# Performance work log

Hardware: AMD Instinct MI355X
Metric: run time of the kernel (lower is better)

## Reference

```python
import jax, jax.numpy as jnp
import numpy as np

POOL = 7
IMG_H, IMG_W = 1024, 1024
CANONICAL = 224.0  # canonical box size used in the FPN level assignment


def _crop_and_resize(fm, boxes, ph, pw):
    """TF-style crop_and_resize (extrapolation_value=0).

    fm: [C, H, W] feature map; boxes: [N, 4] normalized (y1, x1, y2, x2).
    Returns [N, C, ph, pw] bilinearly sampled crops.
    """
    C, H, W = fm.shape
    y1, x1, y2, x2 = boxes[:, 0], boxes[:, 1], boxes[:, 2], boxes[:, 3]
    ty = jnp.arange(ph, dtype=boxes.dtype) / (ph - 1)  # [ph] in [0,1]
    tx = jnp.arange(pw, dtype=boxes.dtype) / (pw - 1)
    ys = (y1[:, None] + (y2 - y1)[:, None] * ty) * (H - 1)  # [N, ph] image coords
    xs = (x1[:, None] + (x2 - x1)[:, None] * tx) * (W - 1)  # [N, pw]
    yy = jnp.broadcast_to(ys[:, :, None], (ys.shape[0], ph, pw))  # [N, ph, pw]
    xx = jnp.broadcast_to(xs[:, None, :], (xs.shape[0], ph, pw))
    y0f = jnp.floor(yy)
    x0f = jnp.floor(xx)
    wy = yy - y0f
    wx = xx - x0f
    y0 = jnp.clip(y0f.astype(jnp.int32), 0, H - 1)
    y1i = jnp.clip(y0 + 1, 0, H - 1)
    x0 = jnp.clip(x0f.astype(jnp.int32), 0, W - 1)
    x1i = jnp.clip(x0 + 1, 0, W - 1)

    def g(yi, xi):
        return fm[:, yi, xi]  # [C, N, ph, pw]

    val = (g(y0, x0) * ((1 - wy) * (1 - wx))[None]
           + g(y0, x1i) * ((1 - wy) * wx)[None]
           + g(y1i, x0) * (wy * (1 - wx))[None]
           + g(y1i, x1i) * (wy * wx)[None])
    # extrapolation_value = 0 for samples outside the feature map
    inb = (yy >= 0) & (yy <= H - 1) & (xx >= 0) & (xx <= W - 1)
    val = jnp.where(inb[None], val, 0.0)
    return jnp.transpose(val, (1, 0, 2, 3))  # [N, C, ph, pw]


def setup_inputs() -> dict:
    key = jax.random.key(0)
    k1, k2, k3, k4, k5, k6, k7, k8 = jax.random.split(key, 8)
    N = 1000
    y1 = jax.random.uniform(k1, (N, 1)) * 0.7
    x1 = jax.random.uniform(k2, (N, 1)) * 0.7
    hh = jax.random.uniform(k3, (N, 1)) * 0.28 + 0.02
    ww = jax.random.uniform(k4, (N, 1)) * 0.28 + 0.02
    boxes = jnp.concatenate([y1, x1, y1 + hh, x1 + ww], axis=1)[None]  # [1,N,4]
    C = 256
    p2 = jax.random.normal(k5, (1, C, 256, 256), dtype=jnp.float32)
    p3 = jax.random.normal(k6, (1, C, 128, 128), dtype=jnp.float32)
    p4 = jax.random.normal(k7, (1, C, 64, 64), dtype=jnp.float32)
    p5 = jax.random.normal(k8, (1, C, 32, 32), dtype=jnp.float32)
    return {"boxes": boxes, "p2": p2, "p3": p3, "p4": p4, "p5": p5}


def reference(boxes, p2, p3, p4, p5):
    boxes = boxes[0]  # squeeze batch, [N,4]
    fms = [p2[0], p3[0], p4[0], p5[0]]  # each [C,H,W]
    y1, x1, y2, x2 = boxes[:, 0:1], boxes[:, 1:2], boxes[:, 2:3], boxes[:, 3:4]
    h = y2 - y1
    w = x2 - x1
    image_area = jnp.asarray(float(IMG_H * IMG_W), dtype=boxes.dtype)
    roi_level = 4 + jnp.log2(jnp.sqrt(h * w) / (CANONICAL / jnp.sqrt(image_area)))
    roi_level = jnp.clip(jnp.round(roi_level), 2, 5).astype(jnp.int32)[:, 0]  # [N]
    # Boxes are detached before cropping in the original (level_boxes.detach()).
    crop_boxes = jax.lax.stop_gradient(boxes)
    out = jnp.zeros((boxes.shape[0], fms[0].shape[0], POOL, POOL), dtype=boxes.dtype)
    for i, level in enumerate(range(2, 6)):
        crop = _crop_and_resize(fms[i], crop_boxes, POOL, POOL)
        sel = (roi_level == level)[:, None, None, None]
        out = out + jnp.where(sel, crop, 0.0)
    return out  # [N, C, POOL, POOL], original box order (sort restores order)
```

## Files before the change

kernel.cpp:

```cpp
#include <hip/hip_runtime.h>

#define POOL 7
#define NCH 256
#define OUT_PER_BOX (NCH * POOL * POOL)
#define PARTS 7
#define PART_SZ (OUT_PER_BOX / PARTS)
#define ITERS (PART_SZ / 256)

#define HW3 16384
#define HW4 4096
#define HW5 1024
#define T3_FLOATS (HW3 * NCH)
#define T4_FLOATS (HW4 * NCH)
#define T5_FLOATS (HW5 * NCH)
#define TILES3 (HW3 / 64 * 4)
#define TILES4 (HW4 / 64 * 4)
#define TILES5 (HW5 / 64 * 4)
#define NTILES (TILES3 + TILES4 + TILES5)

__global__ __launch_bounds__(256) void transpose_kernel(
    const float* __restrict__ p3, const float* __restrict__ p4,
    const float* __restrict__ p5, float* __restrict__ T3,
    float* __restrict__ T4, float* __restrict__ T5)
{
    __shared__ float tile[64][65];
    int bid = blockIdx.x;
    const float* src; float* dst; int HW;
    if (bid < TILES3)                { src = p3; dst = T3; HW = HW3; }
    else if (bid < TILES3 + TILES4)  { bid -= TILES3; src = p4; dst = T4; HW = HW4; }
    else                             { bid -= TILES3 + TILES4; src = p5; dst = T5; HW = HW5; }

    const int ct  = bid & 3;
    const int hwt = bid >> 2;
    const int c0  = ct * 64, hw0 = hwt * 64;
    const int tx  = threadIdx.x & 63, ty = threadIdx.x >> 6;

    #pragma unroll
    for (int r = ty; r < 64; r += 4)
        tile[r][tx] = src[(size_t)(c0 + r) * HW + hw0 + tx];
    __syncthreads();
    #pragma unroll
    for (int r = ty; r < 64; r += 4)
        dst[(size_t)(hw0 + r) * 256 + c0 + tx] = tile[tx][r];
}

__global__ __launch_bounds__(256) void hwc_kernel(
    const float* __restrict__ boxes,
    const float* __restrict__ T3, const float* __restrict__ T4,
    const float* __restrict__ T5, float* __restrict__ out, int nbox)
{
    const int n  = blockIdx.x >> 1;
    const int hb = blockIdx.x & 1;
    if (n >= nbox) return;

    const float by1 = boxes[n * 4 + 0];
    const float bx1 = boxes[n * 4 + 1];
    const float by2 = boxes[n * 4 + 2];
    const float bx2 = boxes[n * 4 + 3];
    const float h = by2 - by1;
    const float w = bx2 - bx1;
    const float lvlf = 4.0f + log2f(sqrtf(h * w) / 0.21875f);
    int lvl = (int)rintf(lvlf);
    lvl = lvl < 2 ? 2 : (lvl > 5 ? 5 : lvl);
    if (lvl == 2) return;

    const float* T; int H;
    if (lvl == 3)      { T = T3; H = 128; }
    else if (lvl == 4) { T = T4; H = 64;  }
    else               { T = T5; H = 32;  }
    const float Hm1 = (float)(H - 1);

    __shared__ float obuf[49][132];
    __shared__ int   s_y0[POOL], s_y1[POOL], s_xb[POOL], s_xcl[POOL];
    __shared__ float s_wy[POOL], s_wx[POOL], s_vy[POOL], s_vx[POOL];

    const int tid = threadIdx.x;
    if (tid < POOL) {
        const float t7 = (float)tid * (1.0f / 6.0f);

        const float yy  = (by1 + h * t7) * Hm1;
        const float y0f = floorf(yy);
        int y0 = (int)y0f; y0 = min(H - 1, max(0, y0));
        s_y0[tid] = y0;
        s_y1[tid] = min(H - 1, y0 + 1);
        s_wy[tid] = yy - y0f;
        s_vy[tid] = (yy >= 0.0f && yy <= Hm1) ? 1.0f : 0.0f;

        const float xx  = (bx1 + w * t7) * Hm1;
        const float x0f = floorf(xx);
        int x0 = (int)x0f; x0 = min(H - 1, max(0, x0));
        s_xb[tid]  = min(x0, H - 2);
        s_xcl[tid] = (x0 == H - 1) ? 1 : 0;
        s_wx[tid]  = xx - x0f;
        s_vx[tid]  = (xx >= 0.0f && xx <= Hm1) ? 1.0f : 0.0f;
    }
    __syncthreads();

    const int wv = tid >> 6;
    const int ln = tid & 63;
    const int cb = hb * 128 + 2 * ln;

    for (int pos = wv; pos < 49; pos += 4) {
        const int py = pos / 7;
        const int px = pos - py * 7;
        const int y0 = s_y0[py], y1 = s_y1[py];
        const int xb = s_xb[px], cl = s_xcl[px];

        const size_t a0 = ((size_t)(y0 * H + xb) << 8) + cb;
        const size_t a1 = ((size_t)(y1 * H + xb) << 8) + cb;
        const float2 A0 = *(const float2*)&T[a0];
        const float2 A1 = *(const float2*)&T[a0 + 256];
        const float2 B0 = *(const float2*)&T[a1];
        const float2 B1 = *(const float2*)&T[a1 + 256];

        const float wy = s_wy[py], wx = s_wx[px];
        const float vv = s_vy[py] * s_vx[px];

        float2 o;
        {
            const float v00 = cl ? A1.x : A0.x;
            const float v01 = A1.x;
            const float v10 = cl ? B1.x : B0.x;
            const float v11 = B1.x;
            const float r0 = v00 + wx * (v01 - v00);
            const float r1 = v10 + wx * (v11 - v10);
            o.x = (r0 + wy * (r1 - r0)) * vv;
        }
        {
            const float v00 = cl ? A1.y : A0.y;
            const float v01 = A1.y;
            const float v10 = cl ? B1.y : B0.y;
            const float v11 = B1.y;
            const float r0 = v00 + wx * (v01 - v00);
            const float r1 = v10 + wx * (v11 - v10);
            o.y = (r0 + wy * (r1 - r0)) * vv;
        }
        *(float2*)&obuf[pos][2 * ln] = o;
    }
    __syncthreads();

    const size_t ob = (size_t)n * OUT_PER_BOX + (size_t)hb * 128 * 49;
    for (int i = tid; i < 128 * 49; i += 256) {
        const int c   = i / 49;
        const int pos = i - c * 49;
        out[ob + i] = obuf[pos][c];
    }
}

__global__ __launch_bounds__(256) void gather2_kernel(
    const float* __restrict__ boxes,
    const float* __restrict__ p2,
    float* __restrict__ out, int nbox)
{
    const int n    = blockIdx.x % nbox;
    const int part = blockIdx.x / nbox;
    const int tid  = threadIdx.x;

    const float by1 = boxes[n * 4 + 0];
    const float bx1 = boxes[n * 4 + 1];
    const float by2 = boxes[n * 4 + 2];
    const float bx2 = boxes[n * 4 + 3];
    const float h = by2 - by1;
    const float w = bx2 - bx1;
    const float lvlf = 4.0f + log2f(sqrtf(h * w) / 0.21875f);
    int lvl = (int)rintf(lvlf);
    lvl = lvl < 2 ? 2 : (lvl > 5 ? 5 : lvl);
    if (lvl != 2) return;

    const float* fm = p2;
    const int H = 256;
    const int HW = 65536;
    const float Hm1 = 255.0f;

    __shared__ int   s_y0[POOL], s_y1[POOL], s_xb[POOL], s_xcl[POOL];
    __shared__ float s_wy[POOL], s_wx[POOL], s_vy[POOL], s_vx[POOL];

    if (tid < POOL) {
        const float t7 = (float)tid * (1.0f / 6.0f);
        const float yy  = (by1 + h * t7) * Hm1;
        const float y0f = floorf(yy);
        int y0 = (int)y0f; y0 = min(H - 1, max(0, y0));
        s_y0[tid] = y0;
        s_y1[tid] = min(H - 1, y0 + 1);
        s_wy[tid] = yy - y0f;
        s_vy[tid] = (yy >= 0.0f && yy <= Hm1) ? 1.0f : 0.0f;
        const float xx  = (bx1 + w * t7) * Hm1;
        const float x0f = floorf(xx);
        int x0 = (int)x0f; x0 = min(H - 1, max(0, x0));
        s_xb[tid]  = min(x0, H - 2);
        s_xcl[tid] = (x0 == H - 1) ? 1 : 0;
        s_wx[tid]  = xx - x0f;
        s_vx[tid]  = (xx >= 0.0f && xx <= Hm1) ? 1.0f : 0.0f;
    }
    __syncthreads();

    const size_t out_base = (size_t)n * OUT_PER_BOX + (size_t)part * PART_SZ;
    const int idx0 = part * PART_SZ + tid;

    float2 q0[ITERS], q1[ITERS];
    #pragma unroll
    for (int i = 0; i < ITERS; ++i) {
        const int idx = idx0 + i * 256;
        const int c  = idx / 49;
        const int r  = idx - c * 49;
        const int py = r / 7;
        const int px = r - py * 7;
        const float* fmc = fm + (size_t)c * HW;
        const int xb = s_xb[px];
        q0[i] = *(const float2*)(fmc + s_y0[py] * H + xb);
        q1[i] = *(const float2*)(fmc + s_y1[py] * H + xb);
    }
    #pragma unroll
    for (int i = 0; i < ITERS; ++i) {
        const int idx = idx0 + i * 256;
        const int c  = idx / 49;
        const int r  = idx - c * 49;
        const int py = r / 7;
        const int px = r - py * 7;
        const float wy = s_wy[py], wx = s_wx[px];
        const int   cl = s_xcl[px];
        const float v00 = cl ? q0[i].y : q0[i].x;
        const float v01 = q0[i].y;
        const float v10 = cl ? q1[i].y : q1[i].x;
        const float v11 = q1[i].y;
        const float r0 = v00 + wx * (v01 - v00);
        const float r1 = v10 + wx * (v11 - v10);
        out[out_base + (size_t)(i * 256 + tid)] =
            (r0 + wy * (r1 - r0)) * s_vy[py] * s_vx[px];
    }
}

__global__ __launch_bounds__(256) void roi_align_flat_kernel(
    const float* __restrict__ boxes,
    const float* __restrict__ p2, const float* __restrict__ p3,
    const float* __restrict__ p4, const float* __restrict__ p5,
    float* __restrict__ out, int nbox)
{
    const int n    = blockIdx.x % nbox;
    const int part = blockIdx.x / nbox;
    const int tid  = threadIdx.x;

    __shared__ int   s_y0[POOL], s_y1[POOL], s_xb[POOL], s_xcl[POOL];
    __shared__ float s_wy[POOL], s_wx[POOL], s_vy[POOL], s_vx[POOL];

    const float by1 = boxes[n * 4 + 0];
    const float bx1 = boxes[n * 4 + 1];
    const float by2 = boxes[n * 4 + 2];
    const float bx2 = boxes[n * 4 + 3];
    const float h = by2 - by1;
    const float w = bx2 - bx1;
    const float lvlf = 4.0f + log2f(sqrtf(h * w) / 0.21875f);
    int lvl = (int)rintf(lvlf);
    lvl = lvl < 2 ? 2 : (lvl > 5 ? 5 : lvl);

    const float* fm;
    int H;
    switch (lvl) {
        case 2:  fm = p2; H = 256; break;
        case 3:  fm = p3; H = 128; break;
        case 4:  fm = p4; H = 64;  break;
        default: fm = p5; H = 32;  break;
    }
    const float Hm1 = (float)(H - 1);

    if (tid < POOL) {
        const float t7 = (float)tid * (1.0f / 6.0f);
        const float yy  = (by1 + h * t7) * Hm1;
        const float y0f = floorf(yy);
        int y0 = (int)y0f; y0 = min(H - 1, max(0, y0));
        s_y0[tid] = y0;
        s_y1[tid] = min(H - 1, y0 + 1);
        s_wy[tid] = yy - y0f;
        s_vy[tid] = (yy >= 0.0f && yy <= Hm1) ? 1.0f : 0.0f;
        const float xx  = (bx1 + w * t7) * Hm1;
        const float x0f = floorf(xx);
        int x0 = (int)x0f; x0 = min(H - 1, max(0, x0));
        s_xb[tid]  = min(x0, H - 2);
        s_xcl[tid] = (x0 == H - 1) ? 1 : 0;
        s_wx[tid]  = xx - x0f;
        s_vx[tid]  = (xx >= 0.0f && xx <= Hm1) ? 1.0f : 0.0f;
    }
    __syncthreads();

    const size_t out_base = (size_t)n * OUT_PER_BOX + (size_t)part * PART_SZ;
    const int idx0 = part * PART_SZ + tid;
    const int HW = H * H;

    float2 q0[ITERS], q1[ITERS];
    #pragma unroll
    for (int i = 0; i < ITERS; ++i) {
        const int idx = idx0 + i * 256;
        const int c  = idx / 49;
        const int r  = idx - c * 49;
        const int py = r / 7;
        const int px = r - py * 7;
        const float* fmc = fm + (size_t)c * HW;
        const int xb = s_xb[px];
        q0[i] = *(const float2*)(fmc + s_y0[py] * H + xb);
        q1[i] = *(const float2*)(fmc + s_y1[py] * H + xb);
    }
    #pragma unroll
    for (int i = 0; i < ITERS; ++i) {
        const int idx = idx0 + i * 256;
        const int c  = idx / 49;
        const int r  = idx - c * 49;
        const int py = r / 7;
        const int px = r - py * 7;
        const float wy = s_wy[py], wx = s_wx[px];
        const int   cl = s_xcl[px];
        const float v00 = cl ? q0[i].y : q0[i].x;
        const float v01 = q0[i].y;
        const float v10 = cl ? q1[i].y : q1[i].x;
        const float v11 = q1[i].y;
        const float r0 = v00 + wx * (v01 - v00);
        const float r1 = v10 + wx * (v11 - v10);
        out[out_base + (size_t)(i * 256 + tid)] =
            (r0 + wy * (r1 - r0)) * s_vy[py] * s_vx[px];
    }
}

extern "C" void kernel_launch(void* const* d_in, const int* in_sizes, int n_in,
                              void* d_out, int out_size, void* d_ws, size_t ws_size,
                              hipStream_t stream) {
    const float* boxes = (const float*)d_in[0];
    const float* p2    = (const float*)d_in[1];
    const float* p3    = (const float*)d_in[2];
    const float* p4    = (const float*)d_in[3];
    const float* p5    = (const float*)d_in[4];
    float* out         = (float*)d_out;

    const int nbox = in_sizes[0] / 4;
    const size_t need = (size_t)(T3_FLOATS + T4_FLOATS + T5_FLOATS) * sizeof(float);

    if (ws_size < need) {
        roi_align_flat_kernel<<<nbox * PARTS, 256, 0, stream>>>(
            boxes, p2, p3, p4, p5, out, nbox);
        return;
    }

    float* T3 = (float*)d_ws;
    float* T4 = T3 + T3_FLOATS;
    float* T5 = T4 + T4_FLOATS;

    transpose_kernel<<<NTILES, 256, 0, stream>>>(p3, p4, p5, T3, T4, T5);
    hwc_kernel<<<2 * nbox, 256, 0, stream>>>(boxes, T3, T4, T5, out, nbox);
    gather2_kernel<<<nbox * PARTS, 256, 0, stream>>>(boxes, p2, out, nbox);
}
```

Baseline: 162.7 us.

## Drop P3 transpose and fuse level kernels into one slotted launch

```diff
diff --git a/kernel.cpp b/kernel.cpp
--- a/kernel.cpp
+++ b/kernel.cpp
@@ -6,29 +6,25 @@
 #define PARTS 7
 #define PART_SZ (OUT_PER_BOX / PARTS)
 #define ITERS (PART_SZ / 256)
-
-#define HW3 16384
+#define SLOTS 9
+
 #define HW4 4096
 #define HW5 1024
-#define T3_FLOATS (HW3 * NCH)
 #define T4_FLOATS (HW4 * NCH)
 #define T5_FLOATS (HW5 * NCH)
-#define TILES3 (HW3 / 64 * 4)
 #define TILES4 (HW4 / 64 * 4)
 #define TILES5 (HW5 / 64 * 4)
-#define NTILES (TILES3 + TILES4 + TILES5)
+#define NTILES (TILES4 + TILES5)
 
 __global__ __launch_bounds__(256) void transpose_kernel(
-    const float* __restrict__ p3, const float* __restrict__ p4,
-    const float* __restrict__ p5, float* __restrict__ T3,
+    const float* __restrict__ p4, const float* __restrict__ p5,
     float* __restrict__ T4, float* __restrict__ T5)
 {
     __shared__ float tile[64][65];
     int bid = blockIdx.x;
     const float* src; float* dst; int HW;
-    if (bid < TILES3)                { src = p3; dst = T3; HW = HW3; }
-    else if (bid < TILES3 + TILES4)  { bid -= TILES3; src = p4; dst = T4; HW = HW4; }
-    else                             { bid -= TILES3 + TILES4; src = p5; dst = T5; HW = HW5; }
+    if (bid < TILES4) { src = p4; dst = T4; HW = HW4; }
+    else              { bid -= TILES4; src = p5; dst = T5; HW = HW5; }
 
     const int ct  = bid & 3;
     const int hwt = bid >> 2;
@@ -44,14 +40,21 @@
         dst[(size_t)(hw0 + r) * 256 + c0 + tx] = tile[tx][r];
 }
 
-__global__ __launch_bounds__(256) void hwc_kernel(
+__global__ __launch_bounds__(256) void fused_kernel(
     const float* __restrict__ boxes,
-    const float* __restrict__ T3, const float* __restrict__ T4,
-    const float* __restrict__ T5, float* __restrict__ out, int nbox)
+    const float* __restrict__ p2, const float* __restrict__ p3,
+    const float* __restrict__ T4, const float* __restrict__ T5,
+    float* __restrict__ out, int nbox)
 {
-    const int n  = blockIdx.x >> 1;
-    const int hb = blockIdx.x & 1;
+    __shared__ float obuf[49][132];
+    __shared__ int   s_y0[POOL], s_y1[POOL], s_xb[POOL], s_xcl[POOL];
+    __shared__ float s_wy[POOL], s_wx[POOL], s_vy[POOL], s_vx[POOL];
+
+    const int bid  = blockIdx.x;
+    const int n    = bid / SLOTS;
+    const int slot = bid - n * SLOTS;
     if (n >= nbox) return;
+    const int tid = threadIdx.x;
 
     const float by1 = boxes[n * 4 + 0];
     const float bx1 = boxes[n * 4 + 1];
@@ -59,121 +62,80 @@
     const float bx2 = boxes[n * 4 + 3];
     const float h = by2 - by1;
     const float w = bx2 - bx1;
+
     const float lvlf = 4.0f + log2f(sqrtf(h * w) / 0.21875f);
     int lvl = (int)rintf(lvlf);
     lvl = lvl < 2 ? 2 : (lvl > 5 ? 5 : lvl);
-    if (lvl == 2) return;
-
-    const float* T; int H;
-    if (lvl == 3)      { T = T3; H = 128; }
-    else if (lvl == 4) { T = T4; H = 64;  }
-    else               { T = T5; H = 32;  }
-    const float Hm1 = (float)(H - 1);
-
-    __shared__ float obuf[49][132];
-    __shared__ int   s_y0[POOL], s_y1[POOL], s_xb[POOL], s_xcl[POOL];
-    __shared__ float s_wy[POOL], s_wx[POOL], s_vy[POOL], s_vx[POOL];
-
-    const int tid = threadIdx.x;
-    if (tid < POOL) {
-        const float t7 = (float)tid * (1.0f / 6.0f);
-
-        const float yy  = (by1 + h * t7) * Hm1;
-        const float y0f = floorf(yy);
-        int y0 = (int)y0f; y0 = min(H - 1, max(0, y0));
-        s_y0[tid] = y0;
-        s_y1[tid] = min(H - 1, y0 + 1);
-        s_wy[tid] = yy - y0f;
-        s_vy[tid] = (yy >= 0.0f && yy <= Hm1) ? 1.0f : 0.0f;
-
-        const float xx  = (bx1 + w * t7) * Hm1;
-        const float x0f = floorf(xx);
-        int x0 = (int)x0f; x0 = min(H - 1, max(0, x0));
-        s_xb[tid]  = min(x0, H - 2);
-        s_xcl[tid] = (x0 == H - 1) ? 1 : 0;
-        s_wx[tid]  = xx - x0f;
-        s_vx[tid]  = (xx >= 0.0f && xx <= Hm1) ? 1.0f : 0.0f;
-    }
-    __syncthreads();
-
-    const int wv = tid >> 6;
-    const int ln = tid & 63;
-    const int cb = hb * 128 + 2 * ln;
-
-    for (int pos = wv; pos < 49; pos += 4) {
-        const int py = pos / 7;
-        const int px = pos - py * 7;
-        const int y0 = s_y0[py], y1 = s_y1[py];
-        const int xb = s_xb[px], cl = s_xcl[px];
-
-        const size_t a0 = ((size_t)(y0 * H + xb) << 8) + cb;
-        const size_t a1 = ((size_t)(y1 * H + xb) << 8) + cb;
-        const float2 A0 = *(const float2*)&T[a0];
-        const float2 A1 = *(const float2*)&T[a0 + 256];
-        const float2 B0 = *(const float2*)&T[a1];
-        const float2 B1 = *(const float2*)&T[a1 + 256];
-
-        const float wy = s_wy[py], wx = s_wx[px];
-        const float vv = s_vy[py] * s_vx[px];
-
-        float2 o;
-        {
-            const float v00 = cl ? A1.x : A0.x;
-            const float v01 = A1.x;
-            const float v10 = cl ? B1.x : B0.x;
-            const float v11 = B1.x;
+
+    if (slot < PARTS) {
+        if (lvl >= 4) return;
+        const float* fm; int H;
+        if (lvl == 2) { fm = p2; H = 256; } else { fm = p3; H = 128; }
+        const float Hm1 = (float)(H - 1);
+        const int part = slot;
+
+        if (tid < POOL) {
+            const float t7 = (float)tid * (1.0f / 6.0f);
+            const float yy  = (by1 + h * t7) * Hm1;
+            const float y0f = floorf(yy);
+            int y0 = (int)y0f; y0 = min(H - 1, max(0, y0));
+            s_y0[tid] = y0;
+            s_y1[tid] = min(H - 1, y0 + 1);
+            s_wy[tid] = yy - y0f;
+            s_vy[tid] = (yy >= 0.0f && yy <= Hm1) ? 1.0f : 0.0f;
+            const float xx  = (bx1 + w * t7) * Hm1;
+            const float x0f = floorf(xx);
+            int x0 = (int)x0f; x0 = min(H - 1, max(0, x0));
+            s_xb[tid]  = min(x0, H - 2);
+            s_xcl[tid] = (x0 == H - 1) ? 1 : 0;
+            s_wx[tid]  = xx - x0f;
+            s_vx[tid]  = (xx >= 0.0f && xx <= Hm1) ? 1.0f : 0.0f;
+        }
+        __syncthreads();
+
+        const size_t out_base = (size_t)n * OUT_PER_BOX + (size_t)part * PART_SZ;
+        const int idx0 = part * PART_SZ + tid;
+        const int HW = H * H;
+
+        float2 q0[ITERS], q1[ITERS];
+        #pragma unroll
+        for (int i = 0; i < ITERS; ++i) {
+            const int idx = idx0 + i * 256;
+            const int c  = idx / 49;
+            const int r  = idx - c * 49;
+            const int py = r / 7;
+            const int px = r - py * 7;
+            const float* fmc = fm + (size_t)c * HW;
+            const int xb = s_xb[px];
+            q0[i] = *(const float2*)(fmc + s_y0[py] * H + xb);
+            q1[i] = *(const float2*)(fmc + s_y1[py] * H + xb);
+        }
+        #pragma unroll
+        for (int i = 0; i < ITERS; ++i) {
+            const int idx = idx0 + i * 256;
+            const int c  = idx / 49;
+            const int r  = idx - c * 49;
+            const int py = r / 7;
+            const int px = r - py * 7;
+            const float wy = s_wy[py], wx = s_wx[px];
+            const int   cl = s_xcl[px];
+            const float v00 = cl ? q0[i].y : q0[i].x;
+            const float v01 = q0[i].y;
+            const float v10 = cl ? q1[i].y : q1[i].x;
+            const float v11 = q1[i].y;
             const float r0 = v00 + wx * (v01 - v00);
             const float r1 = v10 + wx * (v11 - v10);
-            o.x = (r0 + wy * (r1 - r0)) * vv;
-        }
-        {
-            const float v00 = cl ? A1.y : A0.y;
-            const float v01 = A1.y;
-            const float v10 = cl ? B1.y : B0.y;
-            const float v11 = B1.y;
-            const float r0 = v00 + wx * (v01 - v00);
-            const float r1 = v10 + wx * (v11 - v10);
-            o.y = (r0 + wy * (r1 - r0)) * vv;
-        }
-        *(float2*)&obuf[pos][2 * ln] = o;
-    }
-    __syncthreads();
-
-    const size_t ob = (size_t)n * OUT_PER_BOX + (size_t)hb * 128 * 49;
-    for (int i = tid; i < 128 * 49; i += 256) {
-        const int c   = i / 49;
-        const int pos = i - c * 49;
-        out[ob + i] = obuf[pos][c];
-    }
-}
-
-__global__ __launch_bounds__(256) void gather2_kernel(
-    const float* __restrict__ boxes,
-    const float* __restrict__ p2,
-    float* __restrict__ out, int nbox)
-{
-    const int n    = blockIdx.x % nbox;
-    const int part = blockIdx.x / nbox;
-    const int tid  = threadIdx.x;
-
-    const float by1 = boxes[n * 4 + 0];
-    const float bx1 = boxes[n * 4 + 1];
-    const float by2 = boxes[n * 4 + 2];
-    const float bx2 = boxes[n * 4 + 3];
-    const float h = by2 - by1;
-    const float w = bx2 - bx1;
-    const float lvlf = 4.0f + log2f(sqrtf(h * w) / 0.21875f);
-    int lvl = (int)rintf(lvlf);
-    lvl = lvl < 2 ? 2 : (lvl > 5 ? 5 : lvl);
-    if (lvl != 2) return;
-
-    const float* fm = p2;
-    const int H = 256;
-    const int HW = 65536;
-    const float Hm1 = 255.0f;
-
-    __shared__ int   s_y0[POOL], s_y1[POOL], s_xb[POOL], s_xcl[POOL];
-    __shared__ float s_wy[POOL], s_wx[POOL], s_vy[POOL], s_vx[POOL];
+            out[out_base + (size_t)(i * 256 + tid)] =
+                (r0 + wy * (r1 - r0)) * s_vy[py] * s_vx[px];
+        }
+        return;
+    }
+
+    if (lvl <= 3) return;
+    const int hb = slot - PARTS;
+    const float* T; int H;
+    if (lvl == 4) { T = T4; H = 64; } else { T = T5; H = 32; }
+    const float Hm1 = (float)(H - 1);
 
     if (tid < POOL) {
         const float t7 = (float)tid * (1.0f / 6.0f);
@@ -194,8 +156,112 @@
     }
     __syncthreads();
 
+    const int wv = tid >> 6;
+    const int ln = tid & 63;
+    const int cb = hb * 128 + 2 * ln;
+
+    for (int pos = wv; pos < 49; pos += 4) {
+        const int py = pos / 7;
+        const int px = pos - py * 7;
+        const int y0 = s_y0[py], y1 = s_y1[py];
+        const int xb = s_xb[px], cl = s_xcl[px];
+
+        const size_t a0 = ((size_t)(y0 * H + xb) << 8) + cb;
+        const size_t a1 = ((size_t)(y1 * H + xb) << 8) + cb;
+        const float2 A0 = *(const float2*)&T[a0];
+        const float2 A1 = *(const float2*)&T[a0 + 256];
+        const float2 B0 = *(const float2*)&T[a1];
+        const float2 B1 = *(const float2*)&T[a1 + 256];
+
+        const float wy = s_wy[py], wx = s_wx[px];
+        const float vv = s_vy[py] * s_vx[px];
+
+        float2 o;
+        {
+            const float v00 = cl ? A1.x : A0.x;
+            const float v01 = A1.x;
+            const float v10 = cl ? B1.x : B0.x;
+            const float v11 = B1.x;
+            const float r0 = v00 + wx * (v01 - v00);
+            const float r1 = v10 + wx * (v11 - v10);
+            o.x = (r0 + wy * (r1 - r0)) * vv;
+        }
+        {
+            const float v00 = cl ? A1.y : A0.y;
+            const float v01 = A1.y;
+            const float v10 = cl ? B1.y : B0.y;
+            const float v11 = B1.y;
+            const float r0 = v00 + wx * (v01 - v00);
+            const float r1 = v10 + wx * (v11 - v10);
+            o.y = (r0 + wy * (r1 - r0)) * vv;
+        }
+        *(float2*)&obuf[pos][2 * ln] = o;
+    }
+    __syncthreads();
+
+    const size_t ob = (size_t)n * OUT_PER_BOX + (size_t)hb * 128 * 49;
+    for (int i = tid; i < 128 * 49; i += 256) {
+        const int c   = i / 49;
+        const int pos = i - c * 49;
+        out[ob + i] = obuf[pos][c];
+    }
+}
+
+__global__ __launch_bounds__(256) void roi_align_flat_kernel(
+    const float* __restrict__ boxes,
+    const float* __restrict__ p2, const float* __restrict__ p3,
+    const float* __restrict__ p4, const float* __restrict__ p5,
+    float* __restrict__ out, int nbox)
+{
+    const int n    = blockIdx.x % nbox;
+    const int part = blockIdx.x / nbox;
+    const int tid  = threadIdx.x;
+
+    __shared__ int   s_y0[POOL], s_y1[POOL], s_xb[POOL], s_xcl[POOL];
+    __shared__ float s_wy[POOL], s_wx[POOL], s_vy[POOL], s_vx[POOL];
+
+    const float by1 = boxes[n * 4 + 0];
+    const float bx1 = boxes[n * 4 + 1];
+    const float by2 = boxes[n * 4 + 2];
+    const float bx2 = boxes[n * 4 + 3];
+    const float h = by2 - by1;
+    const float w = bx2 - bx1;
+    const float lvlf = 4.0f + log2f(sqrtf(h * w) / 0.21875f);
+    int lvl = (int)rintf(lvlf);
+    lvl = lvl < 2 ? 2 : (lvl > 5 ? 5 : lvl);
+
+    const float* fm;
+    int H;
+    switch (lvl) {
+        case 2:  fm = p2; H = 256; break;
+        case 3:  fm = p3; H = 128; break;
+        case 4:  fm = p4; H = 64;  break;
+        default: fm = p5; H = 32;  break;
+    }
+    const float Hm1 = (float)(H - 1);
+
+    if (tid < POOL) {
+        const float t7 = (float)tid * (1.0f / 6.0f);
+        const float yy  = (by1 + h * t7) * Hm1;
+        const float y0f = floorf(yy);
+        int y0 = (int)y0f; y0 = min(H - 1, max(0, y0));
+        s_y0[tid] = y0;
+        s_y1[tid] = min(H - 1, y0 + 1);
+        s_wy[tid] = yy - y0f;
+        s_vy[tid] = (yy >= 0.0f && yy <= Hm1) ? 1.0f : 0.0f;
+        const float xx  = (bx1 + w * t7) * Hm1;
+        const float x0f = floorf(xx);
+        int x0 = (int)x0f; x0 = min(H - 1, max(0, x0));
+        s_xb[tid]  = min(x0, H - 2);
+        s_xcl[tid] = (x0 == H - 1) ? 1 : 0;
+        s_wx[tid]  = xx - x0f;
+        s_vx[tid]  = (xx >= 0.0f && xx <= Hm1) ? 1.0f : 0.0f;
+    }
+    __syncthreads();
+
     const size_t out_base = (size_t)n * OUT_PER_BOX + (size_t)part * PART_SZ;
     const int idx0 = part * PART_SZ + tid;
+    const int HW = H * H;
 
     float2 q0[ITERS], q1[ITERS];
     #pragma unroll
@@ -230,95 +296,6 @@
     }
 }
 
-__global__ __launch_bounds__(256) void roi_align_flat_kernel(
-    const float* __restrict__ boxes,
-    const float* __restrict__ p2, const float* __restrict__ p3,
-    const float* __restrict__ p4, const float* __restrict__ p5,
-    float* __restrict__ out, int nbox)
-{
-    const int n    = blockIdx.x % nbox;
-    const int part = blockIdx.x / nbox;
-    const int tid  = threadIdx.x;
-
-    __shared__ int   s_y0[POOL], s_y1[POOL], s_xb[POOL], s_xcl[POOL];
-    __shared__ float s_wy[POOL], s_wx[POOL], s_vy[POOL], s_vx[POOL];
-
-    const float by1 = boxes[n * 4 + 0];
-    const float bx1 = boxes[n * 4 + 1];
-    const float by2 = boxes[n * 4 + 2];
-    const float bx2 = boxes[n * 4 + 3];
-    const float h = by2 - by1;
-    const float w = bx2 - bx1;
-    const float lvlf = 4.0f + log2f(sqrtf(h * w) / 0.21875f);
-    int lvl = (int)rintf(lvlf);
-    lvl = lvl < 2 ? 2 : (lvl > 5 ? 5 : lvl);
-
-    const float* fm;
-    int H;
-    switch (lvl) {
-        case 2:  fm = p2; H = 256; break;
-        case 3:  fm = p3; H = 128; break;
-        case 4:  fm = p4; H = 64;  break;
-        default: fm = p5; H = 32;  break;
-    }
-    const float Hm1 = (float)(H - 1);
-
-    if (tid < POOL) {
-        const float t7 = (float)tid * (1.0f / 6.0f);
-        const float yy  = (by1 + h * t7) * Hm1;
-        const float y0f = floorf(yy);
-        int y0 = (int)y0f; y0 = min(H - 1, max(0, y0));
-        s_y0[tid] = y0;
-        s_y1[tid] = min(H - 1, y0 + 1);
-        s_wy[tid] = yy - y0f;
-        s_vy[tid] = (yy >= 0.0f && yy <= Hm1) ? 1.0f : 0.0f;
-        const float xx  = (bx1 + w * t7) * Hm1;
-        const float x0f = floorf(xx);
-        int x0 = (int)x0f; x0 = min(H - 1, max(0, x0));
-        s_xb[tid]  = min(x0, H - 2);
-        s_xcl[tid] = (x0 == H - 1) ? 1 : 0;
-        s_wx[tid]  = xx - x0f;
-        s_vx[tid]  = (xx >= 0.0f && xx <= Hm1) ? 1.0f : 0.0f;
-    }
-    __syncthreads();
-
-    const size_t out_base = (size_t)n * OUT_PER_BOX + (size_t)part * PART_SZ;
-    const int idx0 = part * PART_SZ + tid;
-    const int HW = H * H;
-
-    float2 q0[ITERS], q1[ITERS];
-    #pragma unroll
-    for (int i = 0; i < ITERS; ++i) {
-        const int idx = idx0 + i * 256;
-        const int c  = idx / 49;
-        const int r  = idx - c * 49;
-        const int py = r / 7;
-        const int px = r - py * 7;
-        const float* fmc = fm + (size_t)c * HW;
-        const int xb = s_xb[px];
-        q0[i] = *(const float2*)(fmc + s_y0[py] * H + xb);
-        q1[i] = *(const float2*)(fmc + s_y1[py] * H + xb);
-    }
-    #pragma unroll
-    for (int i = 0; i < ITERS; ++i) {
-        const int idx = idx0 + i * 256;
-        const int c  = idx / 49;
-        const int r  = idx - c * 49;
-        const int py = r / 7;
-        const int px = r - py * 7;
-        const float wy = s_wy[py], wx = s_wx[px];
-        const int   cl = s_xcl[px];
-        const float v00 = cl ? q0[i].y : q0[i].x;
-        const float v01 = q0[i].y;
-        const float v10 = cl ? q1[i].y : q1[i].x;
-        const float v11 = q1[i].y;
-        const float r0 = v00 + wx * (v01 - v00);
-        const float r1 = v10 + wx * (v11 - v10);
-        out[out_base + (size_t)(i * 256 + tid)] =
-            (r0 + wy * (r1 - r0)) * s_vy[py] * s_vx[px];
-    }
-}
-
 extern "C" void kernel_launch(void* const* d_in, const int* in_sizes, int n_in,
                               void* d_out, int out_size, void* d_ws, size_t ws_size,
                               hipStream_t stream) {
@@ -330,7 +307,7 @@
     float* out         = (float*)d_out;
 
     const int nbox = in_sizes[0] / 4;
-    const size_t need = (size_t)(T3_FLOATS + T4_FLOATS + T5_FLOATS) * sizeof(float);
+    const size_t need = (size_t)(T4_FLOATS + T5_FLOATS) * sizeof(float);
 
     if (ws_size < need) {
         roi_align_flat_kernel<<<nbox * PARTS, 256, 0, stream>>>(
@@ -338,11 +315,10 @@
         return;
     }
 
-    float* T3 = (float*)d_ws;
-    float* T4 = T3 + T3_FLOATS;
+    float* T4 = (float*)d_ws;
     float* T5 = T4 + T4_FLOATS;
 
-    transpose_kernel<<<NTILES, 256, 0, stream>>>(p3, p4, p5, T3, T4, T5);
-    hwc_kernel<<<2 * nbox, 256, 0, stream>>>(boxes, T3, T4, T5, out, nbox);
-    gather2_kernel<<<nbox * PARTS, 256, 0, stream>>>(boxes, p2, out, nbox);
+    transpose_kernel<<<NTILES, 256, 0, stream>>>(p4, p5, T4, T5);
+    fused_kernel<<<nbox * SLOTS, 256, 0, stream>>>(
+        boxes, p2, p3, T4, T5, out, nbox);
 }
```

Result: slower. 170.4 us (+4.8%).
